# Kernel tuning notes

Measured on AMD Instinct MI355X. Metric: run time of the kernel, lower is better.

Reference implementation:

```python
import jax, jax.numpy as jnp
import numpy as np


def setup_inputs() -> dict:
    key = jax.random.key(0)
    k1, k2 = jax.random.split(key)
    B, N, M = 8, 8192, 8192
    points1 = jax.random.normal(k1, (B, N, 2), dtype=jnp.float32)
    points2 = jax.random.normal(k2, (B, M, 2), dtype=jnp.float32)
    return {"points1": points1, "points2": points2}


def reference(points1, points2):
    # points1: [B, N, 2], points2: [B, M, 2]
    # Squared pairwise distances via |a|^2 + |b|^2 - 2 a.b  -> [B, N, M]
    p1_sq = jnp.sum(points1 * points1, axis=-1)  # [B, N]
    p2_sq = jnp.sum(points2 * points2, axis=-1)  # [B, M]
    cross = jnp.einsum("bnd,bmd->bnm", points1, points2)  # [B, N, M]
    sqdist = p1_sq[:, :, None] + p2_sq[:, None, :] - 2.0 * cross
    dist1 = jnp.min(sqdist, axis=2)  # [B, N]: NN of each p1 point in p2
    dist2 = jnp.min(sqdist, axis=1)  # [B, M]: NN of each p2 point in p1
    cost = jnp.mean(dist1, axis=-1) + jnp.mean(dist2, axis=-1)  # [B]
    return jnp.sum(cost)
```

## Files before the change

### kernel.cpp

```cpp
#include <hip/hip_runtime.h>


#define BATCH 8
#define NPTS  8192
#define TPB   256
#define IPT   16
#define PPB   (TPB * IPT)
#define TILES (NPTS / PPB)
#define S     16
#define JCH   (NPTS / S)

__global__ __launch_bounds__(TPB, 2)
void chamfer_partial(const float* __restrict__ p1, const float* __restrict__ p2,
                     float* __restrict__ partial ) {
    __shared__ float4 q[JCH];

    int blk = blockIdx.x;
    int split = blk & (S - 1);      blk >>= 4;
    int tile  = blk & (TILES - 1);  blk >>= 1;
    int b     = blk & (BATCH - 1);  blk >>= 3;
    int dir   = blk;

    const float2* a  = (const float2*)(dir ? p2 : p1) + (size_t)b * NPTS;
    const float2* bp = (const float2*)(dir ? p1 : p2) + (size_t)b * NPTS + split * JCH;

    int t = threadIdx.x;

    for (int j = t; j < JCH; j += TPB) {
        float2 v = bp[j];
        q[j] = make_float4(v.x, v.y, fmaf(v.x, v.x, v.y * v.y), 0.0f);
    }

    int pt_base = tile * PPB;
    float xp[IPT], yp[IPT], m[IPT];
#pragma unroll
    for (int k = 0; k < IPT; ++k) {
        float2 v = a[pt_base + k * TPB + t];
        xp[k] = -2.0f * v.x;
        yp[k] = -2.0f * v.y;
        m[k]  = 3.0e38f;
    }

    __syncthreads();

    for (int j = 0; j < JCH; j += 2) {
        float4 q0 = q[j];
        float4 q1 = q[j + 1];
#pragma unroll
        for (int k = 0; k < IPT; ++k) {
            float t0 = fmaf(yp[k], q0.y, fmaf(xp[k], q0.x, q0.z));
            float t1 = fmaf(yp[k], q1.y, fmaf(xp[k], q1.x, q1.z));
            m[k] = fminf(m[k], fminf(t0, t1));
        }
    }

    float* out = partial + ((size_t)(dir * BATCH + b) * S + split) * NPTS + pt_base;
#pragma unroll
    for (int k = 0; k < IPT; ++k)
        out[k * TPB + t] = m[k];
}

__global__ __launch_bounds__(TPB)
void chamfer_reduce(const float* __restrict__ p1, const float* __restrict__ p2,
                    const float* __restrict__ partial, float* __restrict__ out) {
    int gid   = blockIdx.x * TPB + threadIdx.x;
    int point = gid & (NPTS - 1);
    int rest  = gid >> 13;
    int b     = rest & (BATCH - 1);
    int dir   = rest >> 3;

    const float* base = partial + ((size_t)(dir * BATCH + b) * S) * NPTS + point;
    float m = base[0];
#pragma unroll
    for (int s = 1; s < S; ++s)
        m = fminf(m, base[(size_t)s * NPTS]);

    float2 v = ((const float2*)(dir ? p2 : p1))[(size_t)b * NPTS + point];
    float d = m + fmaf(v.x, v.x, v.y * v.y);

#pragma unroll
    for (int off = 32; off > 0; off >>= 1)
        d += __shfl_down(d, off, 64);

    __shared__ float wsum[TPB / 64];
    int lane = threadIdx.x & 63;
    int w    = threadIdx.x >> 6;
    if (lane == 0) wsum[w] = d;
    __syncthreads();
    if (threadIdx.x == 0) {
        float ssum = wsum[0] + wsum[1] + wsum[2] + wsum[3];
        atomicAdd(out, ssum * (1.0f / NPTS));
    }
}

extern "C" void kernel_launch(void* const* d_in, const int* in_sizes, int n_in,
                              void* d_out, int out_size, void* d_ws, size_t ws_size,
                              hipStream_t stream) {
    const float* p1 = (const float*)d_in[0];
    const float* p2 = (const float*)d_in[1];
    float* out      = (float*)d_out;
    float* partial  = (float*)d_ws;

    hipMemsetAsync(d_out, 0, sizeof(float), stream);

    chamfer_partial<<<2 * BATCH * TILES * S, TPB, 0, stream>>>(p1, p2, partial);
    chamfer_reduce<<<2 * BATCH * NPTS / TPB, TPB, 0, stream>>>(p1, p2, partial, out);
}
```

Before: 138.4 us.

## Use packed FP32 FMA and min3 with larger per-thread tiles and deeper split

The inner distance loop now pairs two query points per packed v_pk_fma_f32 via inline asm, and folds the two min operations into one v_min3_f32, to cut VALU instruction count. Each thread now handles 32 points, so one block covers all 8192 points and the tile dimension disappears. The j-split grows to 64 or 32 when the workspace allows, which keeps the block count up. The cost is higher register pressure with occupancy hinted at 4, plus a larger partial buffer and more work in the reduce kernel.

```diff
diff --git a/kernel.cpp b/kernel.cpp
--- a/kernel.cpp
+++ b/kernel.cpp
@@ -4,22 +4,39 @@
 #define BATCH 8
 #define NPTS  8192
 #define TPB   256
-#define IPT   16
-#define PPB   (TPB * IPT)
-#define TILES (NPTS / PPB)
-#define S     16
-#define JCH   (NPTS / S)
+#define IPT   32
+#define HIPT  (IPT / 2)
 
-__global__ __launch_bounds__(TPB, 2)
+__device__ inline float2 pk_fma_blo(float2 a, float2 b, float2 c) {
+    float2 d;
+    asm("v_pk_fma_f32 %0, %1, %2, %3 op_sel:[0,0,0] op_sel_hi:[1,0,0]"
+        : "=v"(d) : "v"(a), "v"(b), "v"(c));
+    return d;
+}
+__device__ inline float2 pk_fma_bhi(float2 a, float2 b, float2 c) {
+    float2 d;
+    asm("v_pk_fma_f32 %0, %1, %2, %3 op_sel:[0,1,0] op_sel_hi:[1,1,1]"
+        : "=v"(d) : "v"(a), "v"(b), "v"(c));
+    return d;
+}
+__device__ inline float min3f(float a, float b, float c) {
+    float d;
+    asm("v_min3_f32 %0, %1, %2, %3" : "=v"(d) : "v"(a), "v"(b), "v"(c));
+    return d;
+}
+
+template <int S>
+__global__ __launch_bounds__(TPB, 4)
 void chamfer_partial(const float* __restrict__ p1, const float* __restrict__ p2,
                      float* __restrict__ partial ) {
+    constexpr int JCH = NPTS / S;
     __shared__ float4 q[JCH];
 
-    int blk = blockIdx.x;
-    int split = blk & (S - 1);      blk >>= 4;
-    int tile  = blk & (TILES - 1);  blk >>= 1;
-    int b     = blk & (BATCH - 1);  blk >>= 3;
-    int dir   = blk;
+    int blk   = blockIdx.x;
+    int split = blk % S;
+    int rest  = blk / S;
+    int b     = rest & (BATCH - 1);
+    int dir   = rest >> 3;
 
     const float2* a  = (const float2*)(dir ? p2 : p1) + (size_t)b * NPTS;
     const float2* bp = (const float2*)(dir ? p1 : p2) + (size_t)b * NPTS + split * JCH;
@@ -31,35 +48,43 @@
         q[j] = make_float4(v.x, v.y, fmaf(v.x, v.x, v.y * v.y), 0.0f);
     }
 
-    int pt_base = tile * PPB;
-    float xp[IPT], yp[IPT], m[IPT];
+    float2 xp[HIPT], yp[HIPT];
+    float  m[IPT];
 #pragma unroll
-    for (int k = 0; k < IPT; ++k) {
-        float2 v = a[pt_base + k * TPB + t];
-        xp[k] = -2.0f * v.x;
-        yp[k] = -2.0f * v.y;
-        m[k]  = 3.0e38f;
+    for (int kk = 0; kk < HIPT; ++kk) {
+        float2 v0 = a[(2 * kk) * TPB + t];
+        float2 v1 = a[(2 * kk + 1) * TPB + t];
+        xp[kk] = make_float2(-2.0f * v0.x, -2.0f * v1.x);
+        yp[kk] = make_float2(-2.0f * v0.y, -2.0f * v1.y);
+        m[2 * kk] = 3.0e38f;
+        m[2 * kk + 1] = 3.0e38f;
     }
 
     __syncthreads();
 
     for (int j = 0; j < JCH; j += 2) {
-        float4 q0 = q[j];
-        float4 q1 = q[j + 1];
+        float4 Q0 = q[j];
+        float4 Q1 = q[j + 1];
+        float2 q0xy = make_float2(Q0.x, Q0.y), q0zw = make_float2(Q0.z, Q0.w);
+        float2 q1xy = make_float2(Q1.x, Q1.y), q1zw = make_float2(Q1.z, Q1.w);
 #pragma unroll
-        for (int k = 0; k < IPT; ++k) {
-            float t0 = fmaf(yp[k], q0.y, fmaf(xp[k], q0.x, q0.z));
-            float t1 = fmaf(yp[k], q1.y, fmaf(xp[k], q1.x, q1.z));
-            m[k] = fminf(m[k], fminf(t0, t1));
+        for (int kk = 0; kk < HIPT; ++kk) {
+            float2 u0 = pk_fma_blo(xp[kk], q0xy, q0zw);
+            float2 t0 = pk_fma_bhi(yp[kk], q0xy, u0);
+            float2 u1 = pk_fma_blo(xp[kk], q1xy, q1zw);
+            float2 t1 = pk_fma_bhi(yp[kk], q1xy, u1);
+            m[2 * kk]     = min3f(m[2 * kk],     t0.x, t1.x);
+            m[2 * kk + 1] = min3f(m[2 * kk + 1], t0.y, t1.y);
         }
     }
 
-    float* out = partial + ((size_t)(dir * BATCH + b) * S + split) * NPTS + pt_base;
+    float* outp = partial + ((size_t)((dir * BATCH + b) * S + split)) * NPTS;
 #pragma unroll
     for (int k = 0; k < IPT; ++k)
-        out[k * TPB + t] = m[k];
+        outp[k * TPB + t] = m[k];
 }
 
+template <int S>
 __global__ __launch_bounds__(TPB)
 void chamfer_reduce(const float* __restrict__ p1, const float* __restrict__ p2,
                     const float* __restrict__ partial, float* __restrict__ out) {
@@ -103,6 +128,16 @@
 
     hipMemsetAsync(d_out, 0, sizeof(float), stream);
 
-    chamfer_partial<<<2 * BATCH * TILES * S, TPB, 0, stream>>>(p1, p2, partial);
-    chamfer_reduce<<<2 * BATCH * NPTS / TPB, TPB, 0, stream>>>(p1, p2, partial, out);
+    auto need = [](int S) { return (size_t)2 * BATCH * S * NPTS * sizeof(float); };
+
+    if (ws_size >= need(64)) {
+        chamfer_partial<64><<<2 * BATCH * 64, TPB, 0, stream>>>(p1, p2, partial);
+        chamfer_reduce<64><<<2 * BATCH * NPTS / TPB, TPB, 0, stream>>>(p1, p2, partial, out);
+    } else if (ws_size >= need(32)) {
+        chamfer_partial<32><<<2 * BATCH * 32, TPB, 0, stream>>>(p1, p2, partial);
+        chamfer_reduce<32><<<2 * BATCH * NPTS / TPB, TPB, 0, stream>>>(p1, p2, partial, out);
+    } else {
+        chamfer_partial<16><<<2 * BATCH * 16, TPB, 0, stream>>>(p1, p2, partial);
+        chamfer_reduce<16><<<2 * BATCH * NPTS / TPB, TPB, 0, stream>>>(p1, p2, partial, out);
+    }
 }
```

After: 144.2 us. 4.2% more time.

## Use v_min3, software-prefetch LDS, split 32 ways, drop memset

Applied to the files above, without the earlier changes.

The inner loop now handles four query points per iteration and loads the next four from LDS before computing on the current four. It folds the minima with the v_min3_f32 instruction through inline asm. The split count becomes a template parameter and rises to 32 when the workspace is large enough, which gives more blocks, less LDS per block and launch bounds of 4 blocks per SM. The output memset is replaced by a zero write inside the first kernel, removing one API call. The risks are extra partial-buffer traffic in the reduce step and higher register pressure under the tighter launch bounds.

```diff
diff --git a/kernel.cpp b/kernel.cpp
--- a/kernel.cpp
+++ b/kernel.cpp
@@ -7,16 +7,25 @@
 #define IPT   16
 #define PPB   (TPB * IPT)
 #define TILES (NPTS / PPB)
-#define S     16
-#define JCH   (NPTS / S)
 
-__global__ __launch_bounds__(TPB, 2)
+__device__ inline float min3f(float a, float b, float c) {
+    float d;
+    asm("v_min3_f32 %0, %1, %2, %3" : "=v"(d) : "v"(a), "v"(b), "v"(c));
+    return d;
+}
+
+template <int S>
+__global__ __launch_bounds__(TPB, 4)
 void chamfer_partial(const float* __restrict__ p1, const float* __restrict__ p2,
-                     float* __restrict__ partial ) {
+                     float* __restrict__ partial ,
+                     float* __restrict__ out_to_zero) {
+    constexpr int JCH = NPTS / S;
     __shared__ float4 q[JCH];
 
-    int blk = blockIdx.x;
-    int split = blk & (S - 1);      blk >>= 4;
+    if (blockIdx.x == 0 && threadIdx.x == 0) *out_to_zero = 0.0f;
+
+    int blk   = blockIdx.x;
+    int split = blk % S;            blk /= S;
     int tile  = blk & (TILES - 1);  blk >>= 1;
     int b     = blk & (BATCH - 1);  blk >>= 3;
     int dir   = blk;
@@ -43,23 +52,37 @@
 
     __syncthreads();
 
-    for (int j = 0; j < JCH; j += 2) {
-        float4 q0 = q[j];
-        float4 q1 = q[j + 1];
+    float4 Q0 = q[0], Q1 = q[1], Q2 = q[2], Q3 = q[3];
+    for (int j = 0; j < JCH - 4; j += 4) {
+        float4 P0 = q[j + 4], P1 = q[j + 5], P2 = q[j + 6], P3 = q[j + 7];
 #pragma unroll
         for (int k = 0; k < IPT; ++k) {
-            float t0 = fmaf(yp[k], q0.y, fmaf(xp[k], q0.x, q0.z));
-            float t1 = fmaf(yp[k], q1.y, fmaf(xp[k], q1.x, q1.z));
-            m[k] = fminf(m[k], fminf(t0, t1));
+            float t0 = fmaf(yp[k], Q0.y, fmaf(xp[k], Q0.x, Q0.z));
+            float t1 = fmaf(yp[k], Q1.y, fmaf(xp[k], Q1.x, Q1.z));
+            float t2 = fmaf(yp[k], Q2.y, fmaf(xp[k], Q2.x, Q2.z));
+            float t3 = fmaf(yp[k], Q3.y, fmaf(xp[k], Q3.x, Q3.z));
+            m[k] = min3f(m[k], t0, t1);
+            m[k] = min3f(m[k], t2, t3);
         }
+        Q0 = P0; Q1 = P1; Q2 = P2; Q3 = P3;
+    }
+#pragma unroll
+    for (int k = 0; k < IPT; ++k) {
+        float t0 = fmaf(yp[k], Q0.y, fmaf(xp[k], Q0.x, Q0.z));
+        float t1 = fmaf(yp[k], Q1.y, fmaf(xp[k], Q1.x, Q1.z));
+        float t2 = fmaf(yp[k], Q2.y, fmaf(xp[k], Q2.x, Q2.z));
+        float t3 = fmaf(yp[k], Q3.y, fmaf(xp[k], Q3.x, Q3.z));
+        m[k] = min3f(m[k], t0, t1);
+        m[k] = min3f(m[k], t2, t3);
     }
 
-    float* out = partial + ((size_t)(dir * BATCH + b) * S + split) * NPTS + pt_base;
+    float* outp = partial + ((size_t)((dir * BATCH + b) * S + split)) * NPTS + pt_base;
 #pragma unroll
     for (int k = 0; k < IPT; ++k)
-        out[k * TPB + t] = m[k];
+        outp[k * TPB + t] = m[k];
 }
 
+template <int S>
 __global__ __launch_bounds__(TPB)
 void chamfer_reduce(const float* __restrict__ p1, const float* __restrict__ p2,
                     const float* __restrict__ partial, float* __restrict__ out) {
@@ -101,8 +124,13 @@
     float* out      = (float*)d_out;
     float* partial  = (float*)d_ws;
 
-    hipMemsetAsync(d_out, 0, sizeof(float), stream);
+    auto need = [](int S) { return (size_t)2 * BATCH * S * NPTS * sizeof(float); };
 
-    chamfer_partial<<<2 * BATCH * TILES * S, TPB, 0, stream>>>(p1, p2, partial);
-    chamfer_reduce<<<2 * BATCH * NPTS / TPB, TPB, 0, stream>>>(p1, p2, partial, out);
+    if (ws_size >= need(32)) {
+        chamfer_partial<32><<<2 * BATCH * TILES * 32, TPB, 0, stream>>>(p1, p2, partial, out);
+        chamfer_reduce<32><<<2 * BATCH * NPTS / TPB, TPB, 0, stream>>>(p1, p2, partial, out);
+    } else {
+        chamfer_partial<16><<<2 * BATCH * TILES * 16, TPB, 0, stream>>>(p1, p2, partial, out);
+        chamfer_reduce<16><<<2 * BATCH * NPTS / TPB, TPB, 0, stream>>>(p1, p2, partial, out);
+    }
 }
```

New measurement: 125.1 us. -9.6%, faster.

## Compute pairwise distances with split-bf16 MFMA and a single pass for both directions

Applied to the files above, without the earlier changes.

Each fp32 coordinate and squared norm is split into three bf16 parts so that one 16x16x32 bf16 MFMA yields the full squared distance, including norms, at close to fp32 accuracy. A single pass now produces both row minima (kept in registers and reduced with shuffles) and column minima (combined through an LDS atomicMin), so the separate second-direction pass is gone. A prep kernel packs the operand tables and also zeroes the output, replacing the memset. In exchange this adds an extra kernel launch, LDS atomics and bf16-split rounding error, and clamps column minima at zero.

```diff
diff --git a/kernel.cpp b/kernel.cpp
--- a/kernel.cpp
+++ b/kernel.cpp
@@ -1,91 +1,189 @@
 #include <hip/hip_runtime.h>
+#include <stdint.h>
 
 
 #define BATCH 8
 #define NPTS  8192
 #define TPB   256
-#define IPT   16
-#define PPB   (TPB * IPT)
-#define TILES (NPTS / PPB)
-#define S     16
-#define JCH   (NPTS / S)
-
-__global__ __launch_bounds__(TPB, 2)
-void chamfer_partial(const float* __restrict__ p1, const float* __restrict__ p2,
-                     float* __restrict__ partial ) {
-    __shared__ float4 q[JCH];
-
-    int blk = blockIdx.x;
-    int split = blk & (S - 1);      blk >>= 4;
-    int tile  = blk & (TILES - 1);  blk >>= 1;
-    int b     = blk & (BATCH - 1);  blk >>= 3;
-    int dir   = blk;
-
-    const float2* a  = (const float2*)(dir ? p2 : p1) + (size_t)b * NPTS;
-    const float2* bp = (const float2*)(dir ? p1 : p2) + (size_t)b * NPTS + split * JCH;
-
-    int t = threadIdx.x;
-
-    for (int j = t; j < JCH; j += TPB) {
-        float2 v = bp[j];
-        q[j] = make_float4(v.x, v.y, fmaf(v.x, v.x, v.y * v.y), 0.0f);
-    }
-
-    int pt_base = tile * PPB;
-    float xp[IPT], yp[IPT], m[IPT];
-#pragma unroll
-    for (int k = 0; k < IPT; ++k) {
-        float2 v = a[pt_base + k * TPB + t];
-        xp[k] = -2.0f * v.x;
-        yp[k] = -2.0f * v.y;
-        m[k]  = 3.0e38f;
-    }
-
-    __syncthreads();
-
-    for (int j = 0; j < JCH; j += 2) {
-        float4 q0 = q[j];
-        float4 q1 = q[j + 1];
-#pragma unroll
-        for (int k = 0; k < IPT; ++k) {
-            float t0 = fmaf(yp[k], q0.y, fmaf(xp[k], q0.x, q0.z));
-            float t1 = fmaf(yp[k], q1.y, fmaf(xp[k], q1.x, q1.z));
-            m[k] = fminf(m[k], fminf(t0, t1));
+#define NTILES 512
+#define NICHUNK 32
+#define NJSPLIT 16
+#define JCH   512
+#define NJT   32
+
+typedef short bf16x8 __attribute__((ext_vector_type(8)));
+typedef float f32x4  __attribute__((ext_vector_type(4)));
+
+__device__ inline float min3f(float a, float b, float c) {
+    float d;
+    asm("v_min3_f32 %0, %1, %2, %3" : "=v"(d) : "v"(a), "v"(b), "v"(c));
+    return d;
+}
+
+__device__ inline uint32_t bf_rtn_u(float v) {
+    uint32_t u = __float_as_uint(v);
+    return (u + 0x7FFFu + ((u >> 16) & 1u)) >> 16;
+}
+__device__ inline void split3(float v, uint32_t& h, uint32_t& m, uint32_t& l) {
+    h = bf_rtn_u(v);
+    float r1 = v - __uint_as_float(h << 16);
+    m = bf_rtn_u(r1);
+    float r2 = r1 - __uint_as_float(m << 16);
+    l = bf_rtn_u(r2);
+}
+
+__global__ void chamfer_prep(const float* __restrict__ p1, const float* __restrict__ p2,
+                             uint4* __restrict__ atab, uint4* __restrict__ btab,
+                             float* __restrict__ out) {
+    int g = blockIdx.x * TPB + threadIdx.x;
+    if (g == 0) *out = 0.0f;
+    int lane = g & 63;
+    int tile = (g >> 6) & (NTILES - 1);
+    int b    = (g >> 15) & (BATCH - 1);
+    int tb   = g >> 18;
+    int m = lane & 15, q = lane >> 4;
+
+    const float2* src = (const float2*)(tb ? p2 : p1);
+    float2 P = src[(size_t)b * NPTS + tile * 16 + m];
+    float s = fmaf(P.x, P.x, P.y * P.y);
+    float x = tb ? -2.0f * P.x : P.x;
+    float y = tb ? -2.0f * P.y : P.y;
+
+    uint32_t xh, xm, xl, yh, ym, yl, sh, sm, sl;
+    split3(x, xh, xm, xl);
+    split3(y, yh, ym, yl);
+    split3(s, sh, sm, sl);
+    const uint32_t ONE = 0x3F80u;
+
+    uint32_t e[8] = {0,0,0,0,0,0,0,0};
+    if (tb == 0) {
+        if (q == 0)      { e[0]=xh;e[1]=xh;e[2]=xm;e[3]=xh;e[4]=xl;e[5]=xm;e[6]=yh;e[7]=yh; }
+        else if (q == 1) { e[0]=ym;e[1]=yh;e[2]=yl;e[3]=ym;e[4]=sh;e[5]=sm;e[6]=sl;e[7]=ONE; }
+        else if (q == 2) { e[0]=ONE;e[1]=ONE; }
+    } else {
+        if (q == 0)      { e[0]=xh;e[1]=xm;e[2]=xh;e[3]=xl;e[4]=xh;e[5]=xm;e[6]=yh;e[7]=ym; }
+        else if (q == 1) { e[0]=yh;e[1]=yl;e[2]=yh;e[3]=ym;e[4]=ONE;e[5]=ONE;e[6]=ONE;e[7]=sh; }
+        else if (q == 2) { e[0]=sm;e[1]=sl; }
+    }
+    uint4 w;
+    w.x = (e[1] << 16) | e[0];
+    w.y = (e[3] << 16) | e[2];
+    w.z = (e[5] << 16) | e[4];
+    w.w = (e[7] << 16) | e[6];
+    (tb ? btab : atab)[((size_t)b * NTILES + tile) * 64 + lane] = w;
+}
+
+__global__ __launch_bounds__(TPB, 3)
+void chamfer_partial(const uint4* __restrict__ atab, const uint4* __restrict__ btab,
+                     float* __restrict__ rowpart ,
+                     float* __restrict__ colpart ) {
+    __shared__ uint4 ldsB[NJT * 64];
+    __shared__ unsigned int colbuf[NJT * 64];
+    __shared__ float rowbuf[TPB];
+
+    int bx = blockIdx.x;
+    int jsplit = bx & (NJSPLIT - 1);
+    int ichunk = (bx >> 4) & (NICHUNK - 1);
+    int b      = bx >> 9;
+
+    int tid  = threadIdx.x;
+    int lane = tid & 63;
+    int w    = tid >> 6;
+
+    const uint4* bsrc = btab + ((size_t)b * NTILES + jsplit * NJT) * 64;
+    for (int idx = tid; idx < NJT * 64; idx += TPB) ldsB[idx] = bsrc[idx];
+    for (int idx = tid; idx < NJT * 64; idx += TPB) colbuf[idx] = 0x7F800000u;
+
+    const uint4* asrc = atab + ((size_t)b * NTILES + ichunk * 16 + w * 4) * 64 + lane;
+    uint4 atmp[4];
+#pragma unroll
+    for (int it = 0; it < 4; ++it) atmp[it] = asrc[it * 64];
+
+    f32x4 zeroc = {0.0f, 0.0f, 0.0f, 0.0f};
+    float accr[16];
+#pragma unroll
+    for (int i2 = 0; i2 < 16; ++i2) accr[i2] = 3.0e38f;
+
+    __syncthreads();
+
+    for (int jt = 0; jt < NJT; ++jt) {
+        bf16x8 bf = *(const bf16x8*)&ldsB[jt * 64 + lane];
+        float accc = 3.0e38f;
+#pragma unroll
+        for (int it = 0; it < 4; ++it) {
+            bf16x8 af = *(const bf16x8*)&atmp[it];
+            f32x4 C = __builtin_amdgcn_mfma_f32_16x16x32_bf16(af, bf, zeroc, 0, 0, 0);
+            accr[it * 4 + 0] = fminf(accr[it * 4 + 0], C[0]);
+            accr[it * 4 + 1] = fminf(accr[it * 4 + 1], C[1]);
+            accr[it * 4 + 2] = fminf(accr[it * 4 + 2], C[2]);
+            accr[it * 4 + 3] = fminf(accr[it * 4 + 3], C[3]);
+            accc = min3f(min3f(accc, C[0], C[1]), C[2], C[3]);
         }
-    }
-
-    float* out = partial + ((size_t)(dir * BATCH + b) * S + split) * NPTS + pt_base;
-#pragma unroll
-    for (int k = 0; k < IPT; ++k)
-        out[k * TPB + t] = m[k];
+        atomicMin(&colbuf[jt * 64 + lane], __float_as_uint(fmaxf(accc, 0.0f)));
+    }
+
+#pragma unroll
+    for (int i2 = 0; i2 < 16; ++i2) {
+        float v = accr[i2];
+        v = fminf(v, __shfl_xor(v, 1, 64));
+        v = fminf(v, __shfl_xor(v, 2, 64));
+        v = fminf(v, __shfl_xor(v, 4, 64));
+        v = fminf(v, __shfl_xor(v, 8, 64));
+        accr[i2] = v;
+    }
+    __syncthreads();
+
+    if ((lane & 15) == 0) {
+        int q = lane >> 4;
+#pragma unroll
+        for (int it = 0; it < 4; ++it)
+#pragma unroll
+            for (int r = 0; r < 4; ++r)
+                rowbuf[w * 64 + it * 16 + q * 4 + r] = accr[it * 4 + r];
+    }
+    for (int idx = tid; idx < NJT * 16; idx += TPB) {
+        int jt = idx >> 4, n = idx & 15;
+        unsigned int v0 = colbuf[jt * 64 + n];
+        unsigned int v1 = colbuf[jt * 64 + 16 + n];
+        unsigned int v2 = colbuf[jt * 64 + 32 + n];
+        unsigned int v3 = colbuf[jt * 64 + 48 + n];
+        unsigned int mn = min(min(v0, v1), min(v2, v3));
+        colpart[((size_t)b * NICHUNK + ichunk) * NPTS + jsplit * JCH + idx] = __uint_as_float(mn);
+    }
+    __syncthreads();
+    rowpart[((size_t)b * NJSPLIT + jsplit) * NPTS + ichunk * 256 + tid] = rowbuf[tid];
 }
 
 __global__ __launch_bounds__(TPB)
-void chamfer_reduce(const float* __restrict__ p1, const float* __restrict__ p2,
-                    const float* __restrict__ partial, float* __restrict__ out) {
-    int gid   = blockIdx.x * TPB + threadIdx.x;
-    int point = gid & (NPTS - 1);
-    int rest  = gid >> 13;
-    int b     = rest & (BATCH - 1);
-    int dir   = rest >> 3;
-
-    const float* base = partial + ((size_t)(dir * BATCH + b) * S) * NPTS + point;
-    float m = base[0];
-#pragma unroll
-    for (int s = 1; s < S; ++s)
-        m = fminf(m, base[(size_t)s * NPTS]);
-
-    float2 v = ((const float2*)(dir ? p2 : p1))[(size_t)b * NPTS + point];
-    float d = m + fmaf(v.x, v.x, v.y * v.y);
-
+void chamfer_reduce(const float* __restrict__ rowpart, const float* __restrict__ colpart,
+                    float* __restrict__ out) {
+    int gid  = blockIdx.x * TPB + threadIdx.x;
+    int pt   = gid & (NPTS - 1);
+    int b    = (gid >> 13) & (BATCH - 1);
+    int side = gid >> 16;
+
+    float m;
+    if (side == 0) {
+        const float* base = rowpart + (size_t)b * NJSPLIT * NPTS + pt;
+        m = base[0];
+#pragma unroll
+        for (int s = 1; s < NJSPLIT; ++s) m = fminf(m, base[(size_t)s * NPTS]);
+    } else {
+        const float* base = colpart + (size_t)b * NICHUNK * NPTS + pt;
+        m = base[0];
+#pragma unroll
+        for (int s = 1; s < NICHUNK; ++s) m = fminf(m, base[(size_t)s * NPTS]);
+    }
+
+    float d = m;
 #pragma unroll
     for (int off = 32; off > 0; off >>= 1)
         d += __shfl_down(d, off, 64);
 
     __shared__ float wsum[TPB / 64];
     int lane = threadIdx.x & 63;
-    int w    = threadIdx.x >> 6;
-    if (lane == 0) wsum[w] = d;
+    int wv   = threadIdx.x >> 6;
+    if (lane == 0) wsum[wv] = d;
     __syncthreads();
     if (threadIdx.x == 0) {
         float ssum = wsum[0] + wsum[1] + wsum[2] + wsum[3];
@@ -98,11 +196,15 @@
                               hipStream_t stream) {
     const float* p1 = (const float*)d_in[0];
     const float* p2 = (const float*)d_in[1];
-    float* out      = (float*)d_out;
-    float* partial  = (float*)d_ws;
-
-    hipMemsetAsync(d_out, 0, sizeof(float), stream);
-
-    chamfer_partial<<<2 * BATCH * TILES * S, TPB, 0, stream>>>(p1, p2, partial);
-    chamfer_reduce<<<2 * BATCH * NPTS / TPB, TPB, 0, stream>>>(p1, p2, partial, out);
-}
+    float* out = (float*)d_out;
+
+    char* ws = (char*)d_ws;
+    uint4* atab    = (uint4*)(ws);
+    uint4* btab    = (uint4*)(ws + (size_t)4 * 1024 * 1024);
+    float* rowpart = (float*)(ws + (size_t)8 * 1024 * 1024);
+    float* colpart = (float*)(ws + (size_t)12 * 1024 * 1024);
+
+    chamfer_prep<<<2048, TPB, 0, stream>>>(p1, p2, atab, btab, out);
+    chamfer_partial<<<BATCH * NICHUNK * NJSPLIT, TPB, 0, stream>>>(atab, btab, rowpart, colpart);
+    chamfer_reduce<<<2 * BATCH * NPTS / TPB, TPB, 0, stream>>>(rowpart, colpart, out);
+}
```

New measurement: 144.6 us. +4.5%, slower.
